# Optimization experiments

Hardware: AMD Instinct MI355X
Metric: run time of the kernel (lower is better)

The kernel has to match this reference:

```python
import jax, jax.numpy as jnp
import numpy as np

IN_F = 8192
OUT_F = 8192
BATCH = 32


def setup_inputs() -> dict:
    key = jax.random.key(0)
    k_x, k_w, k_s = jax.random.split(key, 3)
    x = jax.random.normal(k_x, (BATCH, IN_F), dtype=jnp.float32)
    # int8-valued weights (stored as int32 for portability), range [-128, 127)
    int8_weights = jax.random.randint(k_w, (IN_F, OUT_F), -128, 127, dtype=jnp.int32)
    scaler = jax.random.uniform(k_s, (1,), dtype=jnp.float32)
    return {"x": x, "int8_weights": int8_weights, "scaler": scaler}


def reference(x, int8_weights, scaler):
    # Dequantize the full weight tensor (as the torch module does), then dense matmul.
    fp_weights = int8_weights.astype(jnp.float32) * scaler  # [in, out]
    return jnp.matmul(x, fp_weights)  # [batch, out]
```

## Files before the change

### kernel.cpp

```cpp
#include <hip/hip_runtime.h>


#define IN_F   8192
#define OUT_F  8192
#define BATCH  32
#define KSPLIT 32
#define KCHUNK (IN_F / KSPLIT)

__global__ void prep_x_kernel(const float* __restrict__ x,
                              const float* __restrict__ scaler,
                              float* __restrict__ xt) {
    int i = blockIdx.x * 256 + threadIdx.x;
    int k = i >> 5;
    int b = i & 31;
    xt[i] = x[b * IN_F + k] * scaler[0];
}

__global__ __launch_bounds__(256, 4)
void lq_main_kernel(const int* __restrict__ w,
                    const float* __restrict__ xt,
                    float* __restrict__ out) {
    const int col = blockIdx.x * 256 + threadIdx.x;
    const int k0  = blockIdx.y * KCHUNK;

    float acc[BATCH];
#pragma unroll
    for (int b = 0; b < BATCH; ++b) acc[b] = 0.0f;

    const int*   wp = w  + (size_t)k0 * OUT_F + col;
    const float* xp = xt + (size_t)k0 * BATCH;

#pragma unroll 4
    for (int k = 0; k < KCHUNK; ++k) {
        float wv = (float)wp[(size_t)k * OUT_F];
        const float* xk = xp + k * BATCH;
#pragma unroll
        for (int b = 0; b < BATCH; ++b)
            acc[b] = fmaf(xk[b], wv, acc[b]);
    }

    float* op = out + col;
#pragma unroll
    for (int b = 0; b < BATCH; ++b)
        atomicAdd(op + (size_t)b * OUT_F, acc[b]);
}

extern "C" void kernel_launch(void* const* d_in, const int* in_sizes, int n_in,
                              void* d_out, int out_size, void* d_ws, size_t ws_size,
                              hipStream_t stream) {
    const float* x = (const float*)d_in[0];
    const int*   w = (const int*)d_in[1];
    const float* s = (const float*)d_in[2];
    float* out = (float*)d_out;
    float* xt  = (float*)d_ws;

    hipMemsetAsync(d_out, 0, (size_t)out_size * sizeof(float), stream);

    prep_x_kernel<<<dim3((BATCH * IN_F) / 256), dim3(256), 0, stream>>>(x, s, xt);

    lq_main_kernel<<<dim3(OUT_F / 256, KSPLIT), dim3(256), 0, stream>>>(w, xt, out);
}
```

Before: 375.9 us.

## Stage x tile in LDS and replace atomic split-K with partial-sum reduction

```diff
diff --git a/kernel.cpp b/kernel.cpp
--- a/kernel.cpp
+++ b/kernel.cpp
@@ -19,30 +19,53 @@
 __global__ __launch_bounds__(256, 4)
 void lq_main_kernel(const int* __restrict__ w,
                     const float* __restrict__ xt,
-                    float* __restrict__ out) {
-    const int col = blockIdx.x * 256 + threadIdx.x;
-    const int k0  = blockIdx.y * KCHUNK;
+                    float* __restrict__ part) {
+    __shared__ float4 xs[KCHUNK * (BATCH / 4)];
+    const int tid = threadIdx.x;
+    const int col = blockIdx.x * 256 + tid;
+    const int kc  = blockIdx.y;
+    const int k0  = kc * KCHUNK;
+
+    const float4* xg = (const float4*)(xt + (size_t)k0 * BATCH);
+#pragma unroll
+    for (int j = 0; j < (KCHUNK * BATCH / 4) / 256; ++j)
+        xs[j * 256 + tid] = xg[j * 256 + tid];
+    __syncthreads();
 
     float acc[BATCH];
 #pragma unroll
     for (int b = 0; b < BATCH; ++b) acc[b] = 0.0f;
 
-    const int*   wp = w  + (size_t)k0 * OUT_F + col;
-    const float* xp = xt + (size_t)k0 * BATCH;
+    const int* wp = w + (size_t)k0 * OUT_F + col;
 
-#pragma unroll 4
+#pragma unroll 8
     for (int k = 0; k < KCHUNK; ++k) {
         float wv = (float)wp[(size_t)k * OUT_F];
-        const float* xk = xp + k * BATCH;
+        const float4* xk = &xs[k * (BATCH / 4)];
 #pragma unroll
-        for (int b = 0; b < BATCH; ++b)
-            acc[b] = fmaf(xk[b], wv, acc[b]);
+        for (int q = 0; q < BATCH / 4; ++q) {
+            float4 xv = xk[q];
+            acc[4 * q + 0] = fmaf(xv.x, wv, acc[4 * q + 0]);
+            acc[4 * q + 1] = fmaf(xv.y, wv, acc[4 * q + 1]);
+            acc[4 * q + 2] = fmaf(xv.z, wv, acc[4 * q + 2]);
+            acc[4 * q + 3] = fmaf(xv.w, wv, acc[4 * q + 3]);
+        }
     }
 
-    float* op = out + col;
+    float* pp = part + (size_t)kc * (BATCH * OUT_F) + col;
 #pragma unroll
     for (int b = 0; b < BATCH; ++b)
-        atomicAdd(op + (size_t)b * OUT_F, acc[b]);
+        pp[(size_t)b * OUT_F] = acc[b];
+}
+
+__global__ void reduce_kernel(const float* __restrict__ part,
+                              float* __restrict__ out) {
+    int i = blockIdx.x * 256 + threadIdx.x;
+    float s = 0.0f;
+#pragma unroll
+    for (int c = 0; c < KSPLIT; ++c)
+        s += part[(size_t)c * (BATCH * OUT_F) + i];
+    out[i] = s;
 }
 
 extern "C" void kernel_launch(void* const* d_in, const int* in_sizes, int n_in,
@@ -51,12 +74,13 @@
     const float* x = (const float*)d_in[0];
     const int*   w = (const int*)d_in[1];
     const float* s = (const float*)d_in[2];
-    float* out = (float*)d_out;
-    float* xt  = (float*)d_ws;
-
-    hipMemsetAsync(d_out, 0, (size_t)out_size * sizeof(float), stream);
+    float* out  = (float*)d_out;
+    float* xt   = (float*)d_ws;
+    float* part = (float*)d_ws + (size_t)BATCH * IN_F;
 
     prep_x_kernel<<<dim3((BATCH * IN_F) / 256), dim3(256), 0, stream>>>(x, s, xt);
 
-    lq_main_kernel<<<dim3(OUT_F / 256, KSPLIT), dim3(256), 0, stream>>>(w, xt, out);
+    lq_main_kernel<<<dim3(OUT_F / 256, KSPLIT), dim3(256), 0, stream>>>(w, xt, part);
+
+    reduce_kernel<<<dim3((BATCH * OUT_F) / 256), dim3(256), 0, stream>>>(part, out);
 }
```

New measurement: 378.8 us. Within noise of the previous version (+0.8%).
